# Kernel tuning notes

Measured on AMD Instinct MI355X. Metric: run time of the kernel, lower is better.

## Reference

```python
import jax, jax.numpy as jnp
import numpy as np
import math

N_LEVELS = 8
PLANE_RES = 512
FEAT_DIM = 16
N_VERT = 10
N_SAMPLES = 262144
LEVEL_OFFSET = 0.0


def _projection_matrices():
    # planotic_solid vertices for n_vertices == 10 (half-dodecahedron)
    phi = (1.0 + math.sqrt(5.0)) / 2.0
    verts = np.array([
        [1.0, 1.0, 1.0], [1.0, 1.0, -1.0], [1.0, -1.0, 1.0], [1.0, -1.0, -1.0],
        [0.0, phi, 1.0 / phi], [0.0, phi, -1.0 / phi],
        [1.0 / phi, 0.0, phi], [1.0 / phi, 0.0, -phi],
        [phi, 1.0 / phi, 0.0], [phi, -1.0 / phi, 0.0]], dtype=np.float64)
    verts /= np.linalg.norm(verts, axis=-1, keepdims=True)
    Ps = []
    for a in verts:
        if a[0] != 0 or a[1] != 0:
            p0 = np.array([-a[1], a[0], 0.0])
        else:
            p0 = np.array([0.0, -a[2], a[1]])
        p1 = np.cross(a, p0)
        p0 /= np.linalg.norm(p0)
        p1 /= np.linalg.norm(p1)
        Ps.append(np.stack([p0, p1], axis=0))
    return np.stack(Ps, axis=0).astype(np.float32)  # (V, 2, 3)

P_MATS = _projection_matrices()

# static ripmap geometry: plane (l1, l2) has shape (H = res>>l2, W = res>>l1)
_W = np.array([PLANE_RES >> l for l in range(N_LEVELS)], dtype=np.int32)
_H = _W.copy()
_SIZES = np.array([int(_H[l2]) * int(_W[l1])
                   for l1 in range(N_LEVELS) for l2 in range(N_LEVELS)], dtype=np.int64)
_OFFS = np.concatenate([[0], np.cumsum(_SIZES)[:-1]]).astype(np.int32)


def build_ripmaps_flat(fm):
    """Build the 8x8 anisotropic mip pyramid and pack all planes into one flat buffer.
    fm: (V, H, W, F). Returns (V, total_pixels, F)."""
    flats = []
    base = fm
    for l1 in range(N_LEVELS):
        if l1 > 0:
            base = 0.5 * (base[:, :, 0::2] + base[:, :, 1::2])  # AvgPool (1,2): pool width
        cur = base
        for l2 in range(N_LEVELS):
            if l2 > 0:
                cur = 0.5 * (cur[:, 0::2] + cur[:, 1::2])        # AvgPool (2,1): pool height
            flats.append(cur.reshape(N_VERT, -1, FEAT_DIM))
    return jnp.concatenate(flats, axis=1)


def multi_anisomip_interp(flat, coords, level):
    """flat: (V, T, F) packed ripmaps; coords: (N, V, 2) in [-1, 1];
    level: (N, V, 2) fractional levels in [0, L-1].
    Quadrilinear: bilinear in space x bilinear across the (l1, l2) level grid."""
    W_arr = jnp.asarray(_W)
    H_arr = jnp.asarray(_H)
    off_arr = jnp.asarray(_OFFS)
    vidx = jnp.arange(N_VERT)[None, :]
    lx, ly = level[..., 0], level[..., 1]
    l1f_f = jnp.clip(jnp.floor(lx), 0.0, N_LEVELS - 1)
    l2f_f = jnp.clip(jnp.floor(ly), 0.0, N_LEVELS - 1)
    wx = jnp.clip(lx - l1f_f, 0.0, 1.0)
    wy = jnp.clip(ly - l2f_f, 0.0, 1.0)
    l1f = l1f_f.astype(jnp.int32)
    l2f = l2f_f.astype(jnp.int32)
    l1c = jnp.minimum(l1f + 1, N_LEVELS - 1)
    l2c = jnp.minimum(l2f + 1, N_LEVELS - 1)
    enc = jnp.zeros(coords.shape[:-1] + (FEAT_DIM,), dtype=flat.dtype)
    for l1, wl1 in ((l1f, 1.0 - wx), (l1c, wx)):
        Wl = W_arr[l1]  # (N, V)
        for l2, wl2 in ((l2f, 1.0 - wy), (l2c, wy)):
            Hl = H_arr[l2]
            off = off_arr[l1 * N_LEVELS + l2]
            u = (coords[..., 0] * 0.5 + 0.5) * Wl - 0.5
            v = (coords[..., 1] * 0.5 + 0.5) * Hl - 0.5
            uf = jnp.floor(u)
            vf = jnp.floor(v)
            fu = u - uf
            fv = v - vf
            ix0 = jnp.clip(uf.astype(jnp.int32), 0, Wl - 1)
            ix1 = jnp.clip(uf.astype(jnp.int32) + 1, 0, Wl - 1)
            iy0 = jnp.clip(vf.astype(jnp.int32), 0, Hl - 1)
            iy1 = jnp.clip(vf.astype(jnp.int32) + 1, 0, Hl - 1)
            wl = wl1 * wl2
            for ix, iy, wc in ((ix0, iy0, (1 - fu) * (1 - fv)),
                               (ix1, iy0, fu * (1 - fv)),
                               (ix0, iy1, (1 - fu) * fv),
                               (ix1, iy1, fu * fv)):
                idx = off + iy * Wl + ix  # (N, V) flat pixel index
                enc = enc + (wl * wc)[..., None] * flat[vidx, idx]
    return enc  # (N, V, F)


def setup_inputs() -> dict:
    key = jax.random.key(0)
    k1, k2, k3 = jax.random.split(key, 3)
    means = jax.random.uniform(k1, (N_SAMPLES, 3), minval=-1.0, maxval=1.0, dtype=jnp.float32)
    A = jax.random.normal(k2, (N_SAMPLES, 3, 3), dtype=jnp.float32) * 0.02
    covs = jnp.einsum('nij,nkj->nik', A, A) + 1e-10 * jnp.eye(3, dtype=jnp.float32)
    fm = jax.random.uniform(k3, (N_VERT, PLANE_RES, PLANE_RES, FEAT_DIM),
                            minval=-0.01, maxval=0.01, dtype=jnp.float32)
    return {"means": means, "covs": covs, "fm": fm}


def reference(means, covs, fm):
    P = jnp.asarray(P_MATS)                                   # (V, 2, 3)
    means_proj = jnp.einsum('nd,vcd->nvc', means, P)          # (N, V, 2)
    sig2 = jnp.einsum('vad,nde,vae->nva', P, covs, P)         # diag of P C P^T, (N, V, 2)
    sigmas = jnp.sqrt(jnp.maximum(sig2, 1e-20))
    level = jnp.log2(sigmas) + LEVEL_OFFSET + math.log2(PLANE_RES)
    level = jnp.clip(level, 0.0, N_LEVELS - 1)
    flat = build_ripmaps_flat(fm)
    enc = multi_anisomip_interp(flat, means_proj, level)      # (N, V, F)
    return enc.reshape(means.shape[0], N_VERT * FEAT_DIM)
```

## Files before the change

kernel.cpp:

```cpp
#include <hip/hip_runtime.h>
#include <hip/hip_fp16.h>


#define NV 10
#define FD 16
#define NS 262144
#define PYR_PX 1040400L
#define PYR_BYTES 332928000L
#define DUP0_PX 10404000
#define DUP_VPX 57600
#define OFF_PL 351360000L

__constant__ float c_P[NV][2][3] = {
  {{-0.7071067811865476f, 0.7071067811865476f, 0.0f},
   {-0.4082482904638631f,-0.4082482904638631f, 0.8164965809277261f}},
  {{-0.7071067811865476f, 0.7071067811865476f, 0.0f},
   { 0.4082482904638631f, 0.4082482904638631f, 0.8164965809277261f}},
  {{ 0.7071067811865476f, 0.7071067811865476f, 0.0f},
   {-0.4082482904638631f, 0.4082482904638631f, 0.8164965809277261f}},
  {{ 0.7071067811865476f, 0.7071067811865476f, 0.0f},
   { 0.4082482904638631f,-0.4082482904638631f, 0.8164965809277261f}},
  {{-1.0f, 0.0f, 0.0f},
   { 0.0f,-0.3568220897730899f, 0.9341723589627157f}},
  {{-1.0f, 0.0f, 0.0f},
   { 0.0f, 0.3568220897730899f, 0.9341723589627157f}},
  {{ 0.0f, 1.0f, 0.0f},
   {-0.9341723589627157f, 0.0f, 0.3568220897730899f}},
  {{ 0.0f, 1.0f, 0.0f},
   { 0.9341723589627157f, 0.0f, 0.3568220897730899f}},
  {{-0.3568220897730899f, 0.9341723589627157f, 0.0f},
   { 0.0f, 0.0f, 1.0f}},
  {{ 0.3568220897730899f, 0.9341723589627157f, 0.0f},
   { 0.0f, 0.0f, 1.0f}},
};

__constant__ int c_CW[8] = {0, 512, 768, 896, 960, 992, 1008, 1016};

__device__ __forceinline__ int offp_a(int l1, int l2) {
  return 1044480 - (1020 << (10 - l1)) + ((1024 - (1024 >> l2)) << (9 - l1));
}

__device__ __forceinline__ uint4 havg(uint4 a, uint4 c, __half2 hhalf) {
  uint4 res;
  __half2* rr = (__half2*)&res;
  const __half2* ha = (const __half2*)&a;
  const __half2* hc = (const __half2*)&c;
  #pragma unroll
  for (int j = 0; j < 4; ++j) rr[j] = __hmul2(__hadd2(ha[j], hc[j]), hhalf);
  return res;
}

__global__ __launch_bounds__(256) void build_all(const float* __restrict__ fm,
                                                 __half* __restrict__ pyr)
{
  __shared__ uint4 ldsA[2048];
  __shared__ uint4 ldsB[1024];
  int bid = blockIdx.x;
  int v = bid >> 8;
  int rem = bid & 255;
  int b = rem >> 2;
  int s = rem & 3;
  int t = threadIdx.x;

  __half* bv = pyr + (long)v * PYR_PX * FD;
  uint4* bv4 = (uint4*)bv;
  const __half2 hhalf = __floats2half2_rn(0.5f, 0.5f);

  {
    const float4* src = (const float4*)(fm +
        (((long)v * 512 + b * 8) * 512 + s * 128) * FD);
    uint2* ldsu2 = (uint2*)ldsA;
    uint2* g0 = (uint2*)bv;
    #pragma unroll
    for (int i = 0; i < 16; ++i) {
      int u = t + 256 * i;
      int r = u >> 9;
      int f4 = u & 511;
      int px = f4 >> 2, q = f4 & 3;
      float4 d = src[(long)r * 2048 + f4];
      __half2 h0 = __floats2half2_rn(d.x, d.y);
      __half2 h1 = __floats2half2_rn(d.z, d.w);
      uint2 val;
      val.x = *(unsigned*)&h0; val.y = *(unsigned*)&h1;
      ldsu2[(r * 128 + px) * 4 + q] = val;
      g0[((long)(b * 8 + r) * 512 + s * 128 + px) * 4 + q] = val;
    }
  }
  __syncthreads();

  #pragma unroll
  for (int l1 = 0; l1 < 8; ++l1) {
    uint4* cur = (l1 & 1) ? ldsB : ldsA;
    const int Wc = 128 >> l1;

    if (l1 < 7) {
      uint4* nxt = (l1 & 1) ? ldsA : ldsB;
      const int Wn = Wc >> 1;
      const int units = 8 * Wn * 2;
      const int Wgn = 512 >> (l1 + 1);
      const int colbase = offp_a(l1 + 1, 0) + s * Wn;
      for (int u = t; u < units; u += 256) {
        int k = u & 1;
        int xr = u >> 1;
        int x = xr & (Wn - 1);
        int r = xr >> (6 - l1);
        uint4 a = cur[(r * Wc + 2 * x) * 2 + k];
        uint4 c = cur[(r * Wc + 2 * x + 1) * 2 + k];
        uint4 res = havg(a, c, hhalf);
        nxt[(r * Wn + x) * 2 + k] = res;
        bv4[(long)(colbase + (b * 8 + r) * Wgn + x) * 2 + k] = res;
      }
    }

    {
      const int slots = Wc * 2;
      if (t < slots) {
        int k = t & 1, x = t >> 1;
        const int Wg = 512 >> l1;
        uint4 r0 = cur[(0 * Wc + x) * 2 + k];
        uint4 r1 = cur[(1 * Wc + x) * 2 + k];
        uint4 r2 = cur[(2 * Wc + x) * 2 + k];
        uint4 r3 = cur[(3 * Wc + x) * 2 + k];
        uint4 r4 = cur[(4 * Wc + x) * 2 + k];
        uint4 r5 = cur[(5 * Wc + x) * 2 + k];
        uint4 r6 = cur[(6 * Wc + x) * 2 + k];
        uint4 r7 = cur[(7 * Wc + x) * 2 + k];
        uint4 a0 = havg(r0, r1, hhalf), a1 = havg(r2, r3, hhalf);
        uint4 a2 = havg(r4, r5, hhalf), a3 = havg(r6, r7, hhalf);
        uint4 b0 = havg(a0, a1, hhalf), b1 = havg(a2, a3, hhalf);
        uint4 c0 = havg(b0, b1, hhalf);
        int gx = s * Wc + x;
        long p1 = (long)offp_a(l1, 1) + (long)(b * 4) * Wg + gx;
        bv4[p1 * 2 + k] = a0;
        bv4[(p1 + Wg) * 2 + k] = a1;
        bv4[(p1 + 2 * Wg) * 2 + k] = a2;
        bv4[(p1 + 3 * Wg) * 2 + k] = a3;
        long p2 = (long)offp_a(l1, 2) + (long)(b * 2) * Wg + gx;
        bv4[p2 * 2 + k] = b0;
        bv4[(p2 + Wg) * 2 + k] = b1;
        long p3 = (long)offp_a(l1, 3) + (long)b * Wg + gx;
        bv4[p3 * 2 + k] = c0;
      }
    }
    __syncthreads();
  }
}

template<int L2SRC, int NLEV>
__global__ __launch_bounds__(256) void pool_hN(__half* __restrict__ pyr)
{
  constexpr int R = 1 << NLEV;
  constexpr int HL = 512 >> (L2SRC + NLEV);
  int total = NV * HL * 2040;
  int t = blockIdx.x * 256 + threadIdx.x;
  if (t >= total) return;
  int u = t % 2040;
  int r2 = t / 2040;
  int c = u >> 1, k = u & 1;
  int y = r2 % HL;
  int v = r2 / HL;
  int l1 = 0;
  #pragma unroll
  for (int i = 1; i < 8; ++i) l1 += (c >= c_CW[i]) ? 1 : 0;
  int x = c - c_CW[l1];
  int W = 512 >> l1;
  __half* bv = pyr + (long)v * PYR_PX * FD;
  const __half* src = bv + (long)offp_a(l1, L2SRC) * FD;

  uint4 d[R];
  long base = ((long)(y * R) * W + x) * FD + k * 8;
  #pragma unroll
  for (int r = 0; r < R; ++r)
    d[r] = *(const uint4*)(src + base + (long)r * W * FD);

  const __half2 hhalf = __floats2half2_rn(0.5f, 0.5f);
  #pragma unroll
  for (int lev = 1; lev <= NLEV; ++lev) {
    int cnt = R >> lev;
    __half* dst = bv + (long)offp_a(l1, L2SRC + lev) * FD;
    #pragma unroll
    for (int r = 0; r < cnt; ++r) {
      d[r] = havg(d[2 * r], d[2 * r + 1], hhalf);
      *(uint4*)(dst + (((long)(y * cnt + r)) * W + x) * FD + k * 8) = d[r];
    }
  }
}

__global__ __launch_bounds__(256) void build_dup(__half* __restrict__ pyr)
{
  int cb = blockIdx.y;
  int l1 = 2 + (cb >> 2), l2 = 2 + (cb & 3);
  int W = 512 >> l1, H = 512 >> l2;
  int units = NV * W * H * 2;
  int gx = blockIdx.x * 256 + threadIdx.x;
  if (gx >= units) return;
  int k = gx & 1;
  int p = gx >> 1;
  int x = p & (W - 1);
  int r = p >> (9 - l1);
  int y = r & (H - 1);
  int v = r >> (9 - l2);
  long srcPx = (long)v * PYR_PX + offp_a(l1, l2) + y * W + min(x + 1, W - 1);
  int Ad = 61440 - (245760 >> l1);
  int Bd = 256 - (1024 >> l2);
  long dstPx = (long)DUP0_PX + (long)v * DUP_VPX + Ad + ((Bd + y) << (9 - l1)) + x;
  const uint4* src = (const uint4*)(pyr + srcPx * FD);
  uint4* dst = (uint4*)(pyr + dstPx * FD);
  dst[k] = src[k];
}

__global__ __launch_bounds__(256) void proj_kernel(const float* __restrict__ means,
                                                   const float* __restrict__ covs,
                                                   float4* __restrict__ pl)
{
  int n = blockIdx.x * 256 + threadIdx.x;
  if (n >= NS) return;
  float m0 = means[3 * n], m1 = means[3 * n + 1], m2 = means[3 * n + 2];
  const float* C = covs + 9L * n;
  float c0 = C[0], c1 = C[1], c2 = C[2];
  float c3 = C[3], c4 = C[4], c5 = C[5];
  float c6 = C[6], c7 = C[7], c8 = C[8];
  #pragma unroll
  for (int v = 0; v < NV; ++v) {
    float p00 = c_P[v][0][0], p01 = c_P[v][0][1], p02 = c_P[v][0][2];
    float p10 = c_P[v][1][0], p11 = c_P[v][1][1], p12 = c_P[v][1][2];
    float cx = m0 * p00 + m1 * p01 + m2 * p02;
    float cy = m0 * p10 + m1 * p11 + m2 * p12;
    float t0 = c0 * p00 + c1 * p01 + c2 * p02;
    float t1 = c3 * p00 + c4 * p01 + c5 * p02;
    float t2 = c6 * p00 + c7 * p01 + c8 * p02;
    float s2x = p00 * t0 + p01 * t1 + p02 * t2;
    t0 = c0 * p10 + c1 * p11 + c2 * p12;
    t1 = c3 * p10 + c4 * p11 + c5 * p12;
    t2 = c6 * p10 + c7 * p11 + c8 * p12;
    float s2y = p10 * t0 + p11 * t1 + p12 * t2;
    float lx = 0.5f * log2f(fmaxf(s2x, 1e-20f)) + 9.0f;
    float ly = 0.5f * log2f(fmaxf(s2y, 1e-20f)) + 9.0f;
    lx = fminf(fmaxf(lx, 0.0f), 7.0f);
    ly = fminf(fmaxf(ly, 0.0f), 7.0f);
    pl[(long)v * NS + n] = make_float4(cx, cy, lx, ly);
  }
}

__global__ __launch_bounds__(256) void interp7(const float4* __restrict__ pl,
                                               const __half* __restrict__ pyr,
                                               float* __restrict__ out)
{
  int bid = blockIdx.x;
  int swz = (bid & 7) * 5120 + (bid >> 3);
  int t = swz * 256 + threadIdx.x;
  int q = t & 3;
  int vlow = (t >> 2) & 1;
  int n = (t >> 3) & (NS - 1);
  int v2 = t >> 21;
  int v = v2 * 2 + vlow;

  float4 p = pl[(long)v * NS + n];
  float cx = p.x, cy = p.y, lx = p.z, ly = p.w;
  int l1f = (int)lx, l2f = (int)ly;
  float wx = lx - (float)l1f, wy = ly - (float)l2f;
  int l1c = min(l1f + 1, 7);
  int l2c = min(l2f + 1, 7);

  bool qodd = (q & 1);
  int dupRel = DUP0_PX + v * DUP_VPX - v * 1040400;

  int sh_0 = 9 - l1f;
  int Ar_0 = 1044480 - (1020 << (10 - l1f));
  float u0 = (cx * 0.5f + 0.5f) * (float)(1 << sh_0) - 0.5f;
  float uf0 = floorf(u0);
  float fu0 = u0 - uf0;
  int iu0 = (int)uf0;
  bool e0 = (iu0 < 0) || (iu0 >= (1 << sh_0) - 1);
  int ix_0 = min(max(iu0, 0), (1 << sh_0) - 1);
  float wxl_0 = qodd ? (e0 ? 0.0f : fu0) : (e0 ? 1.0f : 1.0f - fu0);
  int pOdd_0 = ix_0 & 1;
  int Ad_0 = 61440 - (245760 >> l1f);
  int inR1_0 = ((unsigned)(l1f - 2) <= 3u) ? 1 : 0;

  int sh_1 = 9 - l1c;
  int Ar_1 = 1044480 - (1020 << (10 - l1c));
  float u1 = (cx * 0.5f + 0.5f) * (float)(1 << sh_1) - 0.5f;
  float uf1 = floorf(u1);
  float fu1 = u1 - uf1;
  int iu1 = (int)uf1;
  bool e1 = (iu1 < 0) || (iu1 >= (1 << sh_1) - 1);
  int ix_1 = min(max(iu1, 0), (1 << sh_1) - 1);
  float wxl_1 = qodd ? (e1 ? 0.0f : fu1) : (e1 ? 1.0f : 1.0f - fu1);
  int pOdd_1 = ix_1 & 1;
  int Ad_1 = 61440 - (245760 >> l1c);
  int inR1_1 = ((unsigned)(l1c - 2) <= 3u) ? 1 : 0;

  float wl1_0 = 1.0f - wx, wl1_1 = wx;

  int H0 = 512 >> l2f;
  float vv0 = (cy * 0.5f + 0.5f) * (float)H0 - 0.5f;
  float vf0 = floorf(vv0);
  float fv_0 = vv0 - vf0;
  int iv0 = (int)vf0;
  int iy_0 = min(max(iv0, 0), H0 - 1);
  int dy_0 = min(max(iv0 + 1, 0), H0 - 1) - iy_0;
  int Bv_0 = 1024 - (1024 >> l2f);
  int Bd_0 = 256 - (1024 >> l2f);
  int inR2_0 = ((unsigned)(l2f - 2) <= 3u) ? 1 : 0;

  int H1 = 512 >> l2c;
  float vv1 = (cy * 0.5f + 0.5f) * (float)H1 - 0.5f;
  float vf1 = floorf(vv1);
  float fv_1 = vv1 - vf1;
  int iv1 = (int)vf1;
  int iy_1 = min(max(iv1, 0), H1 - 1);
  int dy_1 = min(max(iv1 + 1, 0), H1 - 1) - iy_1;
  int Bv_1 = 1024 - (1024 >> l2c);
  int Bd_1 = 256 - (1024 >> l2c);
  int inR2_1 = ((unsigned)(l2c - 2) <= 3u) ? 1 : 0;

  float wl2_0 = 1.0f - wy, wl2_1 = wy;

  bool s00 = pOdd_0 && inR1_0 && inR2_0;
  int oA = s00 ? (dupRel + Ad_0 + ((Bd_0 + iy_0) << sh_0) + ix_0 - 1)
               : (Ar_0 + ((Bv_0 + iy_0) << sh_0) + ix_0);
  int oB = oA + (dy_0 << sh_0);
  bool s01 = pOdd_0 && inR1_0 && inR2_1;
  int oC = s01 ? (dupRel + Ad_0 + ((Bd_1 + iy_1) << sh_0) + ix_0 - 1)
               : (Ar_0 + ((Bv_1 + iy_1) << sh_0) + ix_0);
  int oD = oC + (dy_1 << sh_0);
  bool s10 = pOdd_1 && inR1_1 && inR2_0;
  int oE = s10 ? (dupRel + Ad_1 + ((Bd_0 + iy_0) << sh_1) + ix_1 - 1)
               : (Ar_1 + ((Bv_0 + iy_0) << sh_1) + ix_1);
  int oF = oE + (dy_0 << sh_1);
  bool s11 = pOdd_1 && inR1_1 && inR2_1;
  int oG = s11 ? (dupRel + Ad_1 + ((Bd_1 + iy_1) << sh_1) + ix_1 - 1)
               : (Ar_1 + ((Bv_1 + iy_1) << sh_1) + ix_1);
  int oH = oG + (dy_1 << sh_1);

  float wb00 = wl1_0 * wl2_0 * wxl_0;
  float wb01 = wl1_0 * wl2_1 * wxl_0;
  float wb10 = wl1_1 * wl2_0 * wxl_1;
  float wb11 = wl1_1 * wl2_1 * wxl_1;
  __half2 wA = __float2half2_rn(wb00 * (1.0f - fv_0));
  __half2 wB = __float2half2_rn(wb00 * fv_0);
  __half2 wC = __float2half2_rn(wb01 * (1.0f - fv_1));
  __half2 wD = __float2half2_rn(wb01 * fv_1);
  __half2 wE = __float2half2_rn(wb10 * (1.0f - fv_0));
  __half2 wF = __float2half2_rn(wb10 * fv_0);
  __half2 wG = __float2half2_rn(wb11 * (1.0f - fv_1));
  __half2 wH = __float2half2_rn(wb11 * fv_1);

  const __half* bvq = pyr + (long)v * PYR_PX * FD + ((q & 1) * 16 + (q >> 1) * 8);

  uint4 dA = *(const uint4*)(bvq + (long)oA * FD);
  uint4 dB = *(const uint4*)(bvq + (long)oB * FD);
  uint4 dC = *(const uint4*)(bvq + (long)oC * FD);
  uint4 dD = *(const uint4*)(bvq + (long)oD * FD);
  uint4 dE = *(const uint4*)(bvq + (long)oE * FD);
  uint4 dF = *(const uint4*)(bvq + (long)oF * FD);
  uint4 dG = *(const uint4*)(bvq + (long)oG * FD);
  uint4 dH = *(const uint4*)(bvq + (long)oH * FD);
  __builtin_amdgcn_sched_barrier(0);

  __half2 z = __float2half2_rn(0.0f);
  __half2 acc0 = z, acc1 = z, acc2 = z, acc3 = z;
  #define ACC8(D, W) { const __half2* hh = (const __half2*)&(D);      \
    acc0 = __hfma2(hh[0], (W), acc0); acc1 = __hfma2(hh[1], (W), acc1); \
    acc2 = __hfma2(hh[2], (W), acc2); acc3 = __hfma2(hh[3], (W), acc3); }
  ACC8(dA, wA) ACC8(dB, wB) ACC8(dC, wC) ACC8(dD, wD)
  ACC8(dE, wE) ACC8(dF, wF) ACC8(dG, wG) ACC8(dH, wH)
  #undef ACC8

  int a0 = *(int*)&acc0, a1 = *(int*)&acc1;
  int a2 = *(int*)&acc2, a3 = *(int*)&acc3;
  int b0 = __shfl_xor(a0, 1), b1 = __shfl_xor(a1, 1);
  int b2 = __shfl_xor(a2, 1), b3 = __shfl_xor(a3, 1);
  acc0 = __hadd2(acc0, *(__half2*)&b0);
  acc1 = __hadd2(acc1, *(__half2*)&b1);
  acc2 = __hadd2(acc2, *(__half2*)&b2);
  acc3 = __hadd2(acc3, *(__half2*)&b3);

  __half2 s0 = qodd ? acc2 : acc0;
  __half2 s1 = qodd ? acc3 : acc1;
  float2 f0 = __half22float2(s0);
  float2 f1 = __half22float2(s1);
  *(float4*)(out + ((long)n * NV + v) * FD + q * 4) =
      make_float4(f0.x, f0.y, f1.x, f1.y);
}

extern "C" void kernel_launch(void* const* d_in, const int* in_sizes, int n_in,
                              void* d_out, int out_size, void* d_ws, size_t ws_size,
                              hipStream_t stream)
{
  const float* means = (const float*)d_in[0];
  const float* covs  = (const float*)d_in[1];
  const float* fm    = (const float*)d_in[2];
  float* out = (float*)d_out;
  __half* pyr = (__half*)d_ws;
  float4* pl  = (float4*)((char*)d_ws + OFF_PL);

  build_all<<<NV * 256, 256, 0, stream>>>(fm, pyr);
  {
    int tB = NV * 8 * 2040;
    pool_hN<3, 3><<<(tB + 255) / 256, 256, 0, stream>>>(pyr);
    int tC = NV * 4 * 2040;
    pool_hN<6, 1><<<(tC + 255) / 256, 256, 0, stream>>>(pyr);
  }
  {
    dim3 g(1280, 16, 1);
    build_dup<<<g, 256, 0, stream>>>(pyr);
  }
  proj_kernel<<<(NS + 255) / 256, 256, 0, stream>>>(means, covs, pl);

  interp7<<<40960, 256, 0, stream>>>(pl, pyr, out);
}
```

Before: 271.2 us.

## Skip fp16 level-0 pyramid store; read base level from fp32 input, two samples per thread

The pyramid build no longer writes the full-resolution (0,0) level to the fp16 workspace. When the interpolation needs the (0,0) level, it reads the original fp32 feature map directly and converts it on the fly. The interpolation kernel also now handles two samples per thread (n and n+N/2), which doubles the loads in flight per thread and halves the grid. This removes a large workspace write, but the fallback path does wider fp32 reads and uses more registers.

```diff
diff --git a/kernel.cpp b/kernel.cpp
--- a/kernel.cpp
+++ b/kernel.cpp
@@ -5,6 +5,7 @@
 #define NV 10
 #define FD 16
 #define NS 262144
+#define HALF_NS 131072
 #define PYR_PX 1040400L
 #define PYR_BYTES 332928000L
 #define DUP0_PX 10404000
@@ -70,20 +71,18 @@
     const float4* src = (const float4*)(fm +
         (((long)v * 512 + b * 8) * 512 + s * 128) * FD);
     uint2* ldsu2 = (uint2*)ldsA;
-    uint2* g0 = (uint2*)bv;
     #pragma unroll
     for (int i = 0; i < 16; ++i) {
       int u = t + 256 * i;
       int r = u >> 9;
       int f4 = u & 511;
-      int px = f4 >> 2, q = f4 & 3;
+      int px = f4 >> 2, qq = f4 & 3;
       float4 d = src[(long)r * 2048 + f4];
       __half2 h0 = __floats2half2_rn(d.x, d.y);
       __half2 h1 = __floats2half2_rn(d.z, d.w);
       uint2 val;
       val.x = *(unsigned*)&h0; val.y = *(unsigned*)&h1;
-      ldsu2[(r * 128 + px) * 4 + q] = val;
-      g0[((long)(b * 8 + r) * 512 + s * 128 + px) * 4 + q] = val;
+      ldsu2[(r * 128 + px) * 4 + qq] = val;
     }
   }
   __syncthreads();
@@ -242,28 +241,23 @@
   }
 }
 
-__global__ __launch_bounds__(256) void interp7(const float4* __restrict__ pl,
-                                               const __half* __restrict__ pyr,
-                                               float* __restrict__ out)
-{
-  int bid = blockIdx.x;
-  int swz = (bid & 7) * 5120 + (bid >> 3);
-  int t = swz * 256 + threadIdx.x;
-  int q = t & 3;
-  int vlow = (t >> 2) & 1;
-  int n = (t >> 3) & (NS - 1);
-  int v2 = t >> 21;
-  int v = v2 * 2 + vlow;
-
-  float4 p = pl[(long)v * NS + n];
+struct Ctx {
+  int oA, oB, oC, oD, oE, oF, oG, oH;
+  __half2 wA, wB, wC, wD, wE, wF, wG, wH;
+  int z00;
+  float fwA, fwB;
+  int ix0, iy0, dy0;
+};
+
+__device__ __forceinline__ Ctx mk_ctx(const float4 p, const bool qodd,
+                                      const int dupRel)
+{
+  Ctx c;
   float cx = p.x, cy = p.y, lx = p.z, ly = p.w;
   int l1f = (int)lx, l2f = (int)ly;
   float wx = lx - (float)l1f, wy = ly - (float)l2f;
   int l1c = min(l1f + 1, 7);
   int l2c = min(l2f + 1, 7);
-
-  bool qodd = (q & 1);
-  int dupRel = DUP0_PX + v * DUP_VPX - v * 1040400;
 
   int sh_0 = 9 - l1f;
   int Ar_0 = 1044480 - (1020 << (10 - l1f));
@@ -318,71 +312,169 @@
   float wl2_0 = 1.0f - wy, wl2_1 = wy;
 
   bool s00 = pOdd_0 && inR1_0 && inR2_0;
-  int oA = s00 ? (dupRel + Ad_0 + ((Bd_0 + iy_0) << sh_0) + ix_0 - 1)
-               : (Ar_0 + ((Bv_0 + iy_0) << sh_0) + ix_0);
-  int oB = oA + (dy_0 << sh_0);
+  c.oA = s00 ? (dupRel + Ad_0 + ((Bd_0 + iy_0) << sh_0) + ix_0 - 1)
+             : (Ar_0 + ((Bv_0 + iy_0) << sh_0) + ix_0);
+  c.oB = c.oA + (dy_0 << sh_0);
   bool s01 = pOdd_0 && inR1_0 && inR2_1;
-  int oC = s01 ? (dupRel + Ad_0 + ((Bd_1 + iy_1) << sh_0) + ix_0 - 1)
-               : (Ar_0 + ((Bv_1 + iy_1) << sh_0) + ix_0);
-  int oD = oC + (dy_1 << sh_0);
+  c.oC = s01 ? (dupRel + Ad_0 + ((Bd_1 + iy_1) << sh_0) + ix_0 - 1)
+             : (Ar_0 + ((Bv_1 + iy_1) << sh_0) + ix_0);
+  c.oD = c.oC + (dy_1 << sh_0);
   bool s10 = pOdd_1 && inR1_1 && inR2_0;
-  int oE = s10 ? (dupRel + Ad_1 + ((Bd_0 + iy_0) << sh_1) + ix_1 - 1)
-               : (Ar_1 + ((Bv_0 + iy_0) << sh_1) + ix_1);
-  int oF = oE + (dy_0 << sh_1);
+  c.oE = s10 ? (dupRel + Ad_1 + ((Bd_0 + iy_0) << sh_1) + ix_1 - 1)
+             : (Ar_1 + ((Bv_0 + iy_0) << sh_1) + ix_1);
+  c.oF = c.oE + (dy_0 << sh_1);
   bool s11 = pOdd_1 && inR1_1 && inR2_1;
-  int oG = s11 ? (dupRel + Ad_1 + ((Bd_1 + iy_1) << sh_1) + ix_1 - 1)
-               : (Ar_1 + ((Bv_1 + iy_1) << sh_1) + ix_1);
-  int oH = oG + (dy_1 << sh_1);
+  c.oG = s11 ? (dupRel + Ad_1 + ((Bd_1 + iy_1) << sh_1) + ix_1 - 1)
+             : (Ar_1 + ((Bv_1 + iy_1) << sh_1) + ix_1);
+  c.oH = c.oG + (dy_1 << sh_1);
 
   float wb00 = wl1_0 * wl2_0 * wxl_0;
   float wb01 = wl1_0 * wl2_1 * wxl_0;
   float wb10 = wl1_1 * wl2_0 * wxl_1;
   float wb11 = wl1_1 * wl2_1 * wxl_1;
-  __half2 wA = __float2half2_rn(wb00 * (1.0f - fv_0));
-  __half2 wB = __float2half2_rn(wb00 * fv_0);
-  __half2 wC = __float2half2_rn(wb01 * (1.0f - fv_1));
-  __half2 wD = __float2half2_rn(wb01 * fv_1);
-  __half2 wE = __float2half2_rn(wb10 * (1.0f - fv_0));
-  __half2 wF = __float2half2_rn(wb10 * fv_0);
-  __half2 wG = __float2half2_rn(wb11 * (1.0f - fv_1));
-  __half2 wH = __float2half2_rn(wb11 * fv_1);
+  c.wA = __float2half2_rn(wb00 * (1.0f - fv_0));
+  c.wB = __float2half2_rn(wb00 * fv_0);
+  c.wC = __float2half2_rn(wb01 * (1.0f - fv_1));
+  c.wD = __float2half2_rn(wb01 * fv_1);
+  c.wE = __float2half2_rn(wb10 * (1.0f - fv_0));
+  c.wF = __float2half2_rn(wb10 * fv_0);
+  c.wG = __float2half2_rn(wb11 * (1.0f - fv_1));
+  c.wH = __float2half2_rn(wb11 * fv_1);
+
+  c.z00 = ((l1f | l2f) == 0) ? 1 : 0;
+  c.fwA = wb00 * (1.0f - fv_0);
+  c.fwB = wb00 * fv_0;
+  c.ix0 = ix_0; c.iy0 = iy_0; c.dy0 = dy_0;
+  if (c.z00) {
+    __half2 z = __float2half2_rn(0.0f);
+    c.wA = z; c.wB = z;
+  }
+  return c;
+}
+
+__global__ __launch_bounds__(256) void interp8(const float4* __restrict__ pl,
+                                               const __half* __restrict__ pyr,
+                                               const float* __restrict__ fm,
+                                               float* __restrict__ out)
+{
+  int bid = blockIdx.x;
+  int swz = (bid & 7) * 2560 + (bid >> 3);
+  int t = swz * 256 + threadIdx.x;
+  int q = t & 3;
+  bool qodd = (q & 1);
+  int vlow = (t >> 2) & 1;
+  int n = (t >> 3) & (HALF_NS - 1);
+  int v2 = t >> 20;
+  int v = v2 * 2 + vlow;
+  int nA = n, nB = n + HALF_NS;
+  int dupRel = DUP0_PX + v * DUP_VPX - v * 1040400;
+
+  float4 pA = pl[(long)v * NS + nA];
+  float4 pB = pl[(long)v * NS + nB];
 
   const __half* bvq = pyr + (long)v * PYR_PX * FD + ((q & 1) * 16 + (q >> 1) * 8);
 
-  uint4 dA = *(const uint4*)(bvq + (long)oA * FD);
-  uint4 dB = *(const uint4*)(bvq + (long)oB * FD);
-  uint4 dC = *(const uint4*)(bvq + (long)oC * FD);
-  uint4 dD = *(const uint4*)(bvq + (long)oD * FD);
-  uint4 dE = *(const uint4*)(bvq + (long)oE * FD);
-  uint4 dF = *(const uint4*)(bvq + (long)oF * FD);
-  uint4 dG = *(const uint4*)(bvq + (long)oG * FD);
-  uint4 dH = *(const uint4*)(bvq + (long)oH * FD);
+  Ctx cA = mk_ctx(pA, qodd, dupRel);
+  uint4 dAA = *(const uint4*)(bvq + (long)cA.oA * FD);
+  uint4 dAB = *(const uint4*)(bvq + (long)cA.oB * FD);
+  uint4 dAC = *(const uint4*)(bvq + (long)cA.oC * FD);
+  uint4 dAD = *(const uint4*)(bvq + (long)cA.oD * FD);
+  uint4 dAE = *(const uint4*)(bvq + (long)cA.oE * FD);
+  uint4 dAF = *(const uint4*)(bvq + (long)cA.oF * FD);
+  uint4 dAG = *(const uint4*)(bvq + (long)cA.oG * FD);
+  uint4 dAH = *(const uint4*)(bvq + (long)cA.oH * FD);
+
+  Ctx cB = mk_ctx(pB, qodd, dupRel);
+  uint4 dBA = *(const uint4*)(bvq + (long)cB.oA * FD);
+  uint4 dBB = *(const uint4*)(bvq + (long)cB.oB * FD);
+  uint4 dBC = *(const uint4*)(bvq + (long)cB.oC * FD);
+  uint4 dBD = *(const uint4*)(bvq + (long)cB.oD * FD);
+  uint4 dBE = *(const uint4*)(bvq + (long)cB.oE * FD);
+  uint4 dBF = *(const uint4*)(bvq + (long)cB.oF * FD);
+  uint4 dBG = *(const uint4*)(bvq + (long)cB.oG * FD);
+  uint4 dBH = *(const uint4*)(bvq + (long)cB.oH * FD);
   __builtin_amdgcn_sched_barrier(0);
 
   __half2 z = __float2half2_rn(0.0f);
-  __half2 acc0 = z, acc1 = z, acc2 = z, acc3 = z;
-  #define ACC8(D, W) { const __half2* hh = (const __half2*)&(D);      \
-    acc0 = __hfma2(hh[0], (W), acc0); acc1 = __hfma2(hh[1], (W), acc1); \
-    acc2 = __hfma2(hh[2], (W), acc2); acc3 = __hfma2(hh[3], (W), acc3); }
-  ACC8(dA, wA) ACC8(dB, wB) ACC8(dC, wC) ACC8(dD, wD)
-  ACC8(dE, wE) ACC8(dF, wF) ACC8(dG, wG) ACC8(dH, wH)
+  __half2 aA0 = z, aA1 = z, aA2 = z, aA3 = z;
+  __half2 aB0 = z, aB1 = z, aB2 = z, aB3 = z;
+  #define ACC8(A0, A1, A2, A3, D, W) { const __half2* hh = (const __half2*)&(D); \
+    A0 = __hfma2(hh[0], (W), A0); A1 = __hfma2(hh[1], (W), A1);                   \
+    A2 = __hfma2(hh[2], (W), A2); A3 = __hfma2(hh[3], (W), A3); }
+  ACC8(aA0,aA1,aA2,aA3, dAA, cA.wA) ACC8(aA0,aA1,aA2,aA3, dAB, cA.wB)
+  ACC8(aA0,aA1,aA2,aA3, dAC, cA.wC) ACC8(aA0,aA1,aA2,aA3, dAD, cA.wD)
+  ACC8(aA0,aA1,aA2,aA3, dAE, cA.wE) ACC8(aA0,aA1,aA2,aA3, dAF, cA.wF)
+  ACC8(aA0,aA1,aA2,aA3, dAG, cA.wG) ACC8(aA0,aA1,aA2,aA3, dAH, cA.wH)
+  ACC8(aB0,aB1,aB2,aB3, dBA, cB.wA) ACC8(aB0,aB1,aB2,aB3, dBB, cB.wB)
+  ACC8(aB0,aB1,aB2,aB3, dBC, cB.wC) ACC8(aB0,aB1,aB2,aB3, dBD, cB.wD)
+  ACC8(aB0,aB1,aB2,aB3, dBE, cB.wE) ACC8(aB0,aB1,aB2,aB3, dBF, cB.wF)
+  ACC8(aB0,aB1,aB2,aB3, dBG, cB.wG) ACC8(aB0,aB1,aB2,aB3, dBH, cB.wH)
   #undef ACC8
 
-  int a0 = *(int*)&acc0, a1 = *(int*)&acc1;
-  int a2 = *(int*)&acc2, a3 = *(int*)&acc3;
-  int b0 = __shfl_xor(a0, 1), b1 = __shfl_xor(a1, 1);
-  int b2 = __shfl_xor(a2, 1), b3 = __shfl_xor(a3, 1);
-  acc0 = __hadd2(acc0, *(__half2*)&b0);
-  acc1 = __hadd2(acc1, *(__half2*)&b1);
-  acc2 = __hadd2(acc2, *(__half2*)&b2);
-  acc3 = __hadd2(acc3, *(__half2*)&b3);
-
-  __half2 s0 = qodd ? acc2 : acc0;
-  __half2 s1 = qodd ? acc3 : acc1;
-  float2 f0 = __half22float2(s0);
-  float2 f1 = __half22float2(s1);
-  *(float4*)(out + ((long)n * NV + v) * FD + q * 4) =
-      make_float4(f0.x, f0.y, f1.x, f1.y);
+  const float* fmv = fm + (long)v * (262144L * FD) + (q >> 1) * 8;
+  if (cA.z00) {
+    int px = min(cA.ix0 + (qodd ? 1 : 0), 511);
+    long o0 = ((long)cA.iy0 * 512 + px) * FD;
+    long o1 = o0 + (long)cA.dy0 * 512 * FD;
+    float4 ga = *(const float4*)(fmv + o0);
+    float4 gb = *(const float4*)(fmv + o0 + 4);
+    float4 ha = *(const float4*)(fmv + o1);
+    float4 hb = *(const float4*)(fmv + o1 + 4);
+    __half2 hw0 = __float2half2_rn(cA.fwA);
+    __half2 hw1 = __float2half2_rn(cA.fwB);
+    aA0 = __hfma2(__floats2half2_rn(ga.x, ga.y), hw0, aA0);
+    aA1 = __hfma2(__floats2half2_rn(ga.z, ga.w), hw0, aA1);
+    aA2 = __hfma2(__floats2half2_rn(gb.x, gb.y), hw0, aA2);
+    aA3 = __hfma2(__floats2half2_rn(gb.z, gb.w), hw0, aA3);
+    aA0 = __hfma2(__floats2half2_rn(ha.x, ha.y), hw1, aA0);
+    aA1 = __hfma2(__floats2half2_rn(ha.z, ha.w), hw1, aA1);
+    aA2 = __hfma2(__floats2half2_rn(hb.x, hb.y), hw1, aA2);
+    aA3 = __hfma2(__floats2half2_rn(hb.z, hb.w), hw1, aA3);
+  }
+  if (cB.z00) {
+    int px = min(cB.ix0 + (qodd ? 1 : 0), 511);
+    long o0 = ((long)cB.iy0 * 512 + px) * FD;
+    long o1 = o0 + (long)cB.dy0 * 512 * FD;
+    float4 ga = *(const float4*)(fmv + o0);
+    float4 gb = *(const float4*)(fmv + o0 + 4);
+    float4 ha = *(const float4*)(fmv + o1);
+    float4 hb = *(const float4*)(fmv + o1 + 4);
+    __half2 hw0 = __float2half2_rn(cB.fwA);
+    __half2 hw1 = __float2half2_rn(cB.fwB);
+    aB0 = __hfma2(__floats2half2_rn(ga.x, ga.y), hw0, aB0);
+    aB1 = __hfma2(__floats2half2_rn(ga.z, ga.w), hw0, aB1);
+    aB2 = __hfma2(__floats2half2_rn(gb.x, gb.y), hw0, aB2);
+    aB3 = __hfma2(__floats2half2_rn(gb.z, gb.w), hw0, aB3);
+    aB0 = __hfma2(__floats2half2_rn(ha.x, ha.y), hw1, aB0);
+    aB1 = __hfma2(__floats2half2_rn(ha.z, ha.w), hw1, aB1);
+    aB2 = __hfma2(__floats2half2_rn(hb.x, hb.y), hw1, aB2);
+    aB3 = __hfma2(__floats2half2_rn(hb.z, hb.w), hw1, aB3);
+  }
+
+  #define XC(A0, A1, A2, A3) {                                   \
+    int x0 = *(int*)&A0, x1 = *(int*)&A1;                        \
+    int x2 = *(int*)&A2, x3 = *(int*)&A3;                        \
+    int y0 = __shfl_xor(x0, 1), y1 = __shfl_xor(x1, 1);          \
+    int y2 = __shfl_xor(x2, 1), y3 = __shfl_xor(x3, 1);          \
+    A0 = __hadd2(A0, *(__half2*)&y0); A1 = __hadd2(A1, *(__half2*)&y1); \
+    A2 = __hadd2(A2, *(__half2*)&y2); A3 = __hadd2(A3, *(__half2*)&y3); }
+  XC(aA0, aA1, aA2, aA3)
+  XC(aB0, aB1, aB2, aB3)
+  #undef XC
+
+  __half2 sA0 = qodd ? aA2 : aA0;
+  __half2 sA1 = qodd ? aA3 : aA1;
+  float2 fA0 = __half22float2(sA0);
+  float2 fA1 = __half22float2(sA1);
+  *(float4*)(out + ((long)nA * NV + v) * FD + q * 4) =
+      make_float4(fA0.x, fA0.y, fA1.x, fA1.y);
+
+  __half2 sB0 = qodd ? aB2 : aB0;
+  __half2 sB1 = qodd ? aB3 : aB1;
+  float2 fB0 = __half22float2(sB0);
+  float2 fB1 = __half22float2(sB1);
+  *(float4*)(out + ((long)nB * NV + v) * FD + q * 4) =
+      make_float4(fB0.x, fB0.y, fB1.x, fB1.y);
 }
 
 extern "C" void kernel_launch(void* const* d_in, const int* in_sizes, int n_in,
@@ -409,5 +501,5 @@
   }
   proj_kernel<<<(NS + 255) / 256, 256, 0, stream>>>(means, covs, pl);
 
-  interp7<<<40960, 256, 0, stream>>>(pl, pyr, out);
-}
+  interp8<<<20480, 256, 0, stream>>>(pl, pyr, fm, out);
+}
```

Result: faster. 251.2 us (-7.3%).
